# Kernel optimization log

Measured on AMD Instinct MI355X. Metric: run time of the kernel, lower is better.

Reference implementation:

```python
import jax, jax.numpy as jnp
import numpy as np

L, H, E, V, BS = 12, 12, 768, 50257, 1024  # layers, heads, n_embd, vocab, block_size
B, T = 2, 1024
D = E // H


def setup_inputs() -> dict:
    key = jax.random.key(0)
    ks = jax.random.split(key, 10)
    s = 0.02
    d = {}
    d["idx"] = jax.random.randint(ks[0], (B, T), 0, V)
    d["targets"] = jax.random.randint(ks[1], (B, T), 0, V)
    # embeddings (wte tied with lm_head)
    d["wte"] = (jax.random.normal(ks[2], (V, E)) * s).astype(jnp.float32)
    d["wpe"] = (jax.random.normal(ks[3], (BS, E)) * s).astype(jnp.float32)
    # stacked per-layer params; Linear weights stored [in, out] (= torch W.T)
    d["ln1_w"] = jnp.ones((L, E), jnp.float32)
    d["ln1_b"] = jnp.zeros((L, E), jnp.float32)
    d["attn_w"] = (jax.random.normal(ks[4], (L, E, 3 * E)) * s).astype(jnp.float32)
    d["attn_b"] = jnp.zeros((L, 3 * E), jnp.float32)
    d["proj_w"] = (jax.random.normal(ks[5], (L, E, E)) * s).astype(jnp.float32)
    d["proj_b"] = jnp.zeros((L, E), jnp.float32)
    d["ln2_w"] = jnp.ones((L, E), jnp.float32)
    d["ln2_b"] = jnp.zeros((L, E), jnp.float32)
    d["fc_w"] = (jax.random.normal(ks[6], (L, E, 4 * E)) * s).astype(jnp.float32)
    d["fc_b"] = jnp.zeros((L, 4 * E), jnp.float32)
    d["fcproj_w"] = (jax.random.normal(ks[7], (L, 4 * E, E)) * s).astype(jnp.float32)
    d["fcproj_b"] = jnp.zeros((L, E), jnp.float32)
    d["lnf_w"] = jnp.ones((E,), jnp.float32)
    d["lnf_b"] = jnp.zeros((E,), jnp.float32)
    return d


def _ln(x, w, b, eps=1e-5):
    m = jnp.mean(x, -1, keepdims=True)
    v = jnp.mean(jnp.square(x - m), -1, keepdims=True)
    return (x - m) * jax.lax.rsqrt(v + eps) * w + b


def _block(x, p, mask):
    l1w, l1b, aw, ab, pw, pb, l2w, l2b, fw, fb, fpw, fpb = p
    Bx, Tx, C = x.shape
    # causal self-attention (explicit QK^T + mask + softmax + AV, as in source)
    qkv = _ln(x, l1w, l1b) @ aw + ab                       # [B,T,3E]
    q, k, v = jnp.split(qkv, 3, axis=-1)
    q = q.reshape(Bx, Tx, H, D).transpose(0, 2, 1, 3)       # [B,H,T,D]
    k = k.reshape(Bx, Tx, H, D).transpose(0, 2, 1, 3)
    v = v.reshape(Bx, Tx, H, D).transpose(0, 2, 1, 3)
    att = jnp.einsum('bhqd,bhkd->bhqk', q, k) * (1.0 / np.sqrt(D))
    att = jnp.where(mask, att, -jnp.inf)
    att = jax.nn.softmax(att, axis=-1)
    y = jnp.einsum('bhqk,bhkd->bhqd', att, v)
    y = y.transpose(0, 2, 1, 3).reshape(Bx, Tx, C)
    x = x + y @ pw + pb
    # MLP with tanh-approx GELU
    h = jax.nn.gelu(_ln(x, l2w, l2b) @ fw + fb, approximate=True)
    x = x + h @ fpw + fpb
    return x


def reference(idx, targets, wte, wpe, ln1_w, ln1_b, attn_w, attn_b, proj_w, proj_b,
              ln2_w, ln2_b, fc_w, fc_b, fcproj_w, fcproj_b, lnf_w, lnf_b):
    Tq = idx.shape[1]
    x = wte[idx] + wpe[:Tq]                                 # [B,T,E]
    mask = jnp.tril(jnp.ones((Tq, Tq), dtype=bool))

    def step(x, p):
        return _block(x, p, mask), None

    layer_params = (ln1_w, ln1_b, attn_w, attn_b, proj_w, proj_b,
                    ln2_w, ln2_b, fc_w, fc_b, fcproj_w, fcproj_b)
    x, _ = jax.lax.scan(step, x, layer_params)
    x = _ln(x, lnf_w, lnf_b)
    logits = x @ wte.T                                      # tied lm_head, [B,T,V]
    logp = jax.nn.log_softmax(logits, axis=-1)
    nll = -jnp.take_along_axis(logp, targets[..., None], axis=-1)[..., 0]
    loss = jnp.mean(nll)
    return logits, loss
```

## Files before the change

### kernel.cpp

```cpp
#include <hip/hip_runtime.h>
#include <hip/hip_bf16.h>
#include <math.h>

#define LNUM 12
#define HNUM 12
#define EDIM 768
#define VDIM 50257
#define BDIM 2
#define TDIM 1024
#define BT (BDIM*TDIM)
#define E3 (3*EDIM)
#define E4 (4*EDIM)
#define NPB (2*((VDIM+127)/128))

typedef __bf16 bf16x8 __attribute__((ext_vector_type(8)));
typedef __bf16 bf16x4 __attribute__((ext_vector_type(4)));
typedef float f32x4 __attribute__((ext_vector_type(4)));

__device__ __forceinline__ float gelu_f(float x) {
    float u = 0.7978845608028654f * (x + 0.044715f * x * x * x);
    return 0.5f * x * (1.0f + tanhf(u));
}

__device__ __forceinline__ void gl16(const void* g, void* l) {
    __builtin_amdgcn_global_load_lds(
        (const __attribute__((address_space(1))) unsigned int*)g,
        (__attribute__((address_space(3))) unsigned int*)l,
        16, 0, 0);
}

__global__ __launch_bounds__(256) void embed_kernel(
    const int* __restrict__ idx, const float* __restrict__ wte,
    const float* __restrict__ wpe, float* __restrict__ x)
{
    const int row = blockIdx.x;
    const int t = row % TDIM;
    const int tok = idx[row];
    const float* we = wte + (size_t)tok * EDIM;
    const float* pe = wpe + (size_t)t * EDIM;
    float* xr = x + (size_t)row * EDIM;
    for (int e = threadIdx.x; e < EDIM; e += 256) xr[e] = we[e] + pe[e];
}

__global__ __launch_bounds__(256) void ln_kernel(
    const float* __restrict__ in, const float* __restrict__ w,
    const float* __restrict__ b, __bf16* __restrict__ out)
{
    const int row = blockIdx.x * 4 + (threadIdx.x >> 6);
    const int lane = threadIdx.x & 63;
    const float4* xr = (const float4*)(in + (size_t)row * EDIM);
    float4 a0 = xr[lane], a1 = xr[64 + lane], a2 = xr[128 + lane];
    float s = a0.x + a0.y + a0.z + a0.w + a1.x + a1.y + a1.z + a1.w
            + a2.x + a2.y + a2.z + a2.w;
    #pragma unroll
    for (int off = 32; off; off >>= 1) s += __shfl_xor(s, off);
    const float mean = s * (1.0f / EDIM);
    float4 d0 = make_float4(a0.x - mean, a0.y - mean, a0.z - mean, a0.w - mean);
    float4 d1 = make_float4(a1.x - mean, a1.y - mean, a1.z - mean, a1.w - mean);
    float4 d2 = make_float4(a2.x - mean, a2.y - mean, a2.z - mean, a2.w - mean);
    float v = d0.x*d0.x + d0.y*d0.y + d0.z*d0.z + d0.w*d0.w
            + d1.x*d1.x + d1.y*d1.y + d1.z*d1.z + d1.w*d1.w
            + d2.x*d2.x + d2.y*d2.y + d2.z*d2.z + d2.w*d2.w;
    #pragma unroll
    for (int off = 32; off; off >>= 1) v += __shfl_xor(v, off);
    const float inv = rsqrtf(v * (1.0f / EDIM) + 1e-5f);
    const float4* w4 = (const float4*)w;
    const float4* b4 = (const float4*)b;
    __bf16* orow = out + (size_t)row * EDIM;
    #pragma unroll
    for (int c = 0; c < 3; ++c) {
        float4 dd = c == 0 ? d0 : (c == 1 ? d1 : d2);
        float4 ww = w4[c * 64 + lane], bb = b4[c * 64 + lane];
        bf16x4 o;
        o[0] = (__bf16)(dd.x * inv * ww.x + bb.x);
        o[1] = (__bf16)(dd.y * inv * ww.y + bb.y);
        o[2] = (__bf16)(dd.z * inv * ww.z + bb.z);
        o[3] = (__bf16)(dd.w * inv * ww.w + bb.w);
        *(bf16x4*)(orow + c * 256 + lane * 4) = o;
    }
}

__global__ __launch_bounds__(256) void convt_kernel(
    const float* __restrict__ in, __bf16* __restrict__ out, int K, int N)
{
    in  += (size_t)blockIdx.z * K * N;
    out += (size_t)blockIdx.z * K * N;
    __shared__ float t[32][33];
    const int n0 = blockIdx.x * 32, k0 = blockIdx.y * 32;
    const int tx = threadIdx.x & 31, ty = threadIdx.x >> 5;
    #pragma unroll
    for (int r = ty; r < 32; r += 8)
        t[r][tx] = in[(size_t)(k0 + r) * N + n0 + tx];
    __syncthreads();
    #pragma unroll
    for (int r = ty; r < 32; r += 8)
        out[(size_t)(n0 + r) * K + k0 + tx] = (__bf16)t[tx][r];
}

__global__ __launch_bounds__(256) void cvt_kernel(
    const float* __restrict__ in, __bf16* __restrict__ out, long n4)
{
    for (long i = blockIdx.x * 256L + threadIdx.x; i < n4; i += (long)gridDim.x * 256L) {
        float4 v = ((const float4*)in)[i];
        out[i * 4 + 0] = (__bf16)v.x;
        out[i * 4 + 1] = (__bf16)v.y;
        out[i * 4 + 2] = (__bf16)v.z;
        out[i * 4 + 3] = (__bf16)v.w;
    }
}

template<int BM, int BN, int BK, bool BIAS, bool GELU_, bool RES_, bool OUTBF, bool NGUARD, bool LOGITS>
__global__ __launch_bounds__(256, 2) void mgemm(
    const __bf16* __restrict__ A, const __bf16* __restrict__ Bt,
    const float* __restrict__ bias, const float* __restrict__ res,
    void* __restrict__ Cout, float* __restrict__ part, int M, int N, int K)
{
    constexpr int WM = BM / 2, WN = BN / 2;
    constexpr int FM = WM / 16, FN = WN / 16;
    constexpr int KS = BK / 32;
    constexpr int TBA = BM * BK * 2;
    constexpr int TBB = BN * BK * 2;
    constexpr int rA = TBA / 4096, rB = TBB / 4096;
    constexpr int RPI = 2048 / BK;
    constexpr int CPR = BK / 8;
    __shared__ __align__(16) __bf16 As[3 * BM * BK];
    __shared__ __align__(16) __bf16 Bs[3 * BN * BK];
    const int tid = threadIdx.x;
    const int lane = tid & 63;
    const int wave = tid >> 6;
    const int wr = wave >> 1, wc = wave & 1;

    int bm, bn;
    if (LOGITS) {
        const int wg = blockIdx.x;
        bm = (wg >> 3) & 7;
        bn = (wg & 7) + ((wg >> 6) << 3);
        if (bn * BN >= N) return;
    } else { bm = blockIdx.y; bn = blockIdx.x; }
    const int m0 = bm * BM;
    const int n0 = bn * BN;

    const int srow = tid / CPR;
    const int skey = (BK == 32) ? ((srow >> 1) & 3) : (srow & 7);
    const int c0 = (tid % CPR) ^ skey;

    const __bf16* gA = A + (size_t)(m0 + srow) * K + c0 * 8;
    const __bf16* gB[rB];
    #pragma unroll
    for (int r = 0; r < rB; ++r) {
        int nr = n0 + srow + r * RPI;
        if (NGUARD) nr = nr < N ? nr : N - 1;
        gB[r] = Bt + (size_t)nr * K + c0 * 8;
    }

    const int fr = lane & 15;
    const int g = lane >> 4;
    const int fkey = (BK == 32) ? ((fr >> 1) & 3) : (fr & 7);

    f32x4 acc[FM][FN];
    #pragma unroll
    for (int i = 0; i < FM; i++)
        #pragma unroll
        for (int j = 0; j < FN; j++) acc[i][j] = (f32x4){0.f, 0.f, 0.f, 0.f};

    const int nt = K / BK;

    auto stage = [&](int kk, int b) {
        #pragma unroll
        for (int r = 0; r < rA; ++r)
            gl16(gA + (size_t)r * RPI * K + kk, (char*)As + b * TBA + r * 4096 + tid * 16);
        #pragma unroll
        for (int r = 0; r < rB; ++r)
            gl16(gB[r] + kk, (char*)Bs + b * TBB + r * 4096 + tid * 16);
    };

    stage(0, 0);
    if (nt > 1) stage(BK, 1);

    int b0 = 0, b1 = 1, b2 = 2;
    for (int t = 0; t < nt; ++t) {
        if (t + 1 < nt) {
            static_assert(rA + rB == 4 || rA + rB == 6, "vmcnt literal");
            if constexpr (rA + rB == 4) asm volatile("s_waitcnt vmcnt(4)" ::: "memory");
            else                        asm volatile("s_waitcnt vmcnt(6)" ::: "memory");
        } else {
            asm volatile("s_waitcnt vmcnt(0)" ::: "memory");
        }
        asm volatile("s_barrier" ::: "memory");
        if (t + 2 < nt) stage((t + 2) * BK, b2);

        const char* pa = (const char*)As + b0 * TBA;
        const char* pb = (const char*)Bs + b0 * TBB;
        bf16x8 af[FM][KS], bfr[FN][KS];
        #pragma unroll
        for (int i = 0; i < FM; i++)
            #pragma unroll
            for (int kc = 0; kc < KS; kc++)
                af[i][kc] = *(const bf16x8*)(pa + (wr * WM + i * 16 + fr) * (2 * BK)
                                                + (((kc * 4 + g) ^ fkey) << 4));
        #pragma unroll
        for (int j = 0; j < FN; j++)
            #pragma unroll
            for (int kc = 0; kc < KS; kc++)
                bfr[j][kc] = *(const bf16x8*)(pb + (wc * WN + j * 16 + fr) * (2 * BK)
                                                 + (((kc * 4 + g) ^ fkey) << 4));
        #pragma unroll
        for (int kc = 0; kc < KS; kc++)
            #pragma unroll
            for (int i = 0; i < FM; i++)
                #pragma unroll
                for (int j = 0; j < FN; j++)
                    acc[i][j] = __builtin_amdgcn_mfma_f32_16x16x32_bf16(af[i][kc], bfr[j][kc], acc[i][j], 0, 0, 0);
        const int tmp = b0; b0 = b1; b1 = b2; b2 = tmp;
    }

    const int crow = g * 4;
    if (LOGITS) {
        const int bn2 = bn * 2 + wc;
        #pragma unroll
        for (int i = 0; i < FM; i++) {
            #pragma unroll
            for (int r = 0; r < 4; r++) {
                const int m = m0 + wr * WM + i * 16 + crow + r;
                float se = 0.f;
                #pragma unroll
                for (int j = 0; j < FN; j++) {
                    const int n = n0 + wc * WN + j * 16 + fr;
                    if (n < N) {
                        float v = acc[i][j][r];
                        ((float*)Cout)[(size_t)m * N + n] = v;
                        se += __expf(v);
                    }
                }
                se += __shfl_xor(se, 1); se += __shfl_xor(se, 2);
                se += __shfl_xor(se, 4); se += __shfl_xor(se, 8);
                if (fr == 0) part[(size_t)m * NPB + bn2] = se;
            }
        }
    } else {
        #pragma unroll
        for (int i = 0; i < FM; i++) {
            #pragma unroll
            for (int r = 0; r < 4; r++) {
                const int m = m0 + wr * WM + i * 16 + crow + r;
                #pragma unroll
                for (int j = 0; j < FN; j++) {
                    const int n = n0 + wc * WN + j * 16 + fr;
                    if (!NGUARD || n < N) {
                        float v = acc[i][j][r];
                        if (BIAS) v += bias[n];
                        if (GELU_) v = gelu_f(v);
                        if (RES_) v += res[(size_t)m * N + n];
                        if (OUTBF) ((__bf16*)Cout)[(size_t)m * N + n] = (__bf16)v;
                        else       ((float*)Cout)[(size_t)m * N + n] = v;
                    }
                }
            }
        }
    }
}

__global__ __launch_bounds__(256) void fattn_kernel(
    const __bf16* __restrict__ qkv, __bf16* __restrict__ y)
{
    const int bq = blockIdx.x, h = blockIdx.y, b = blockIdx.z;
    const int tid = threadIdx.x, lane = tid & 63, w = tid >> 6;
    const int fr = lane & 15, g = lane >> 4;

    __shared__ __align__(16) __bf16 Ks[64 * 64];
    __shared__ __align__(16) __bf16 Vt[64 * 64];
    __shared__ __align__(16) __bf16 Ps[4][16 * 64];

    const __bf16* base = qkv + (size_t)b * TDIM * E3;
    const int q0w = bq * 64 + w * 16;

    bf16x8 qf[2];
    {
        const __bf16* qp = base + (size_t)(q0w + fr) * E3 + h * 64 + g * 8;
        qf[0] = *(const bf16x8*)qp;
        qf[1] = *(const bf16x8*)(qp + 32);
    }

    const int r0 = tid >> 3, ch = tid & 7;
    bf16x8 kr[2], vr[2];

    #pragma unroll
    for (int it = 0; it < 2; ++it) {
        const int row = it * 32 + r0;
        const __bf16* gp = base + (size_t)row * E3 + EDIM + h * 64 + ch * 8;
        kr[it] = *(const bf16x8*)gp;
        vr[it] = *(const bf16x8*)(gp + EDIM);
    }
    #pragma unroll
    for (int it = 0; it < 2; ++it) {
        const int row = it * 32 + r0;
        *(bf16x8*)(Ks + row * 64 + ((ch ^ (row & 7)) << 3)) = kr[it];
        #pragma unroll
        for (int j = 0; j < 8; ++j) {
            const int d = ch * 8 + j;
            const int key = ((d >> 3) ^ d) & 7;
            Vt[d * 64 + ((((row >> 3) ^ key) << 3) + (row & 7))] = vr[it][j];
        }
    }
    __syncthreads();

    float m[4] = {-1e30f, -1e30f, -1e30f, -1e30f};
    float l[4] = {0.f, 0.f, 0.f, 0.f};
    f32x4 acc[4];
    #pragma unroll
    for (int jd = 0; jd < 4; ++jd) acc[jd] = (f32x4){0.f, 0.f, 0.f, 0.f};

    for (int kt = 0; kt <= bq; ++kt) {
        if (kt < bq) {
            const int k1 = (kt + 1) * 64;
            #pragma unroll
            for (int it = 0; it < 2; ++it) {
                const int row = it * 32 + r0;
                const __bf16* gp = base + (size_t)(k1 + row) * E3 + EDIM + h * 64 + ch * 8;
                kr[it] = *(const bf16x8*)gp;
                vr[it] = *(const bf16x8*)(gp + EDIM);
            }
        }

        const int k0 = kt * 64;
        f32x4 s[4];
        #pragma unroll
        for (int jf = 0; jf < 4; ++jf) {
            const int krow = jf * 16 + fr;
            f32x4 sv = (f32x4){0.f, 0.f, 0.f, 0.f};
            #pragma unroll
            for (int kc = 0; kc < 2; ++kc) {
                bf16x8 kf = *(const bf16x8*)(Ks + krow * 64 + (((kc * 4 + g) ^ (fr & 7)) << 3));
                sv = __builtin_amdgcn_mfma_f32_16x16x32_bf16(qf[kc], kf, sv, 0, 0, 0);
            }
            s[jf] = sv;
        }
        #pragma unroll
        for (int jf = 0; jf < 4; ++jf)
            #pragma unroll
            for (int r = 0; r < 4; ++r) s[jf][r] *= 0.125f;
        if (kt == bq) {
            #pragma unroll
            for (int jf = 0; jf < 4; ++jf) {
                const int k = k0 + jf * 16 + fr;
                #pragma unroll
                for (int r = 0; r < 4; ++r) {
                    const int q = q0w + g * 4 + r;
                    if (k > q) s[jf][r] = -1e30f;
                }
            }
        }

        #pragma unroll
        for (int r = 0; r < 4; ++r) {
            float mx = fmaxf(fmaxf(s[0][r], s[1][r]), fmaxf(s[2][r], s[3][r]));
            mx = fmaxf(mx, __shfl_xor(mx, 1));
            mx = fmaxf(mx, __shfl_xor(mx, 2));
            mx = fmaxf(mx, __shfl_xor(mx, 4));
            mx = fmaxf(mx, __shfl_xor(mx, 8));
            const float mn = fmaxf(m[r], mx);
            const float sc2 = __expf(m[r] - mn);
            m[r] = mn;
            float rs = 0.f;
            #pragma unroll
            for (int jf = 0; jf < 4; ++jf) {
                const float p = __expf(s[jf][r] - mn);
                s[jf][r] = p;
                rs += p;
            }
            rs += __shfl_xor(rs, 1);
            rs += __shfl_xor(rs, 2);
            rs += __shfl_xor(rs, 4);
            rs += __shfl_xor(rs, 8);
            l[r] = l[r] * sc2 + rs;
            #pragma unroll
            for (int jd = 0; jd < 4; ++jd) acc[jd][r] *= sc2;
        }

        __bf16* pw = &Ps[w][0];
        #pragma unroll
        for (int jf = 0; jf < 4; ++jf) {
            const int chp = jf * 2 + (fr >> 3);
            #pragma unroll
            for (int r = 0; r < 4; ++r) {
                const int row = g * 4 + r;
                pw[row * 64 + (((chp ^ (row & 7)) << 3) + (fr & 7))] = (__bf16)s[jf][r];
            }
        }
        asm volatile("s_waitcnt lgkmcnt(0)" ::: "memory");
        bf16x8 pa[2];
        #pragma unroll
        for (int kc = 0; kc < 2; ++kc)
            pa[kc] = *(const bf16x8*)(pw + fr * 64 + (((kc * 4 + g) ^ (fr & 7)) << 3));

        #pragma unroll
        for (int jd = 0; jd < 4; ++jd) {
            const int d = jd * 16 + fr;
            const int key = ((d >> 3) ^ d) & 7;
            #pragma unroll
            for (int kc = 0; kc < 2; ++kc) {
                bf16x8 vf = *(const bf16x8*)(Vt + d * 64 + (((kc * 4 + g) ^ key) << 3));
                acc[jd] = __builtin_amdgcn_mfma_f32_16x16x32_bf16(pa[kc], vf, acc[jd], 0, 0, 0);
            }
        }

        if (kt < bq) {
            __syncthreads();
            #pragma unroll
            for (int it = 0; it < 2; ++it) {
                const int row = it * 32 + r0;
                *(bf16x8*)(Ks + row * 64 + ((ch ^ (row & 7)) << 3)) = kr[it];
                #pragma unroll
                for (int j = 0; j < 8; ++j) {
                    const int d = ch * 8 + j;
                    const int key = ((d >> 3) ^ d) & 7;
                    Vt[d * 64 + ((((row >> 3) ^ key) << 3) + (row & 7))] = vr[it][j];
                }
            }
            __syncthreads();
        }
    }

    #pragma unroll
    for (int r = 0; r < 4; ++r) {
        const float inv = 1.0f / l[r];
        const int q = q0w + g * 4 + r;
        __bf16* yp = y + ((size_t)(b * TDIM + q)) * EDIM + h * 64;
        #pragma unroll
        for (int jd = 0; jd < 4; ++jd)
            yp[jd * 16 + fr] = (__bf16)(acc[jd][r] * inv);
    }
}

__global__ __launch_bounds__(256) void lsefin_kernel(
    const float* __restrict__ part, const float* __restrict__ logits,
    const int* __restrict__ targets, float* __restrict__ rr)
{
    const int row = blockIdx.x, tid = threadIdx.x;
    float s = 0.f;
    for (int j = tid; j < NPB; j += 256) s += part[(size_t)row * NPB + j];
    #pragma unroll
    for (int off = 32; off; off >>= 1) s += __shfl_xor(s, off);
    __shared__ float red[4];
    if ((tid & 63) == 0) red[tid >> 6] = s;
    __syncthreads();
    if (tid == 0) {
        float S = red[0] + red[1] + red[2] + red[3];
        rr[row] = logf(S) - logits[(size_t)row * VDIM + targets[row]];
    }
}

__global__ __launch_bounds__(256) void loss_reduce_kernel(
    const float* __restrict__ rr, float* __restrict__ out)
{
    const int tid = threadIdx.x;
    float s = 0.f;
    for (int i = tid; i < BT; i += 256) s += rr[i];
    #pragma unroll
    for (int off = 32; off; off >>= 1) s += __shfl_xor(s, off);
    __shared__ float red[4];
    if ((tid & 63) == 0) red[tid >> 6] = s;
    __syncthreads();
    if (tid == 0) out[0] = (red[0] + red[1] + red[2] + red[3]) * (1.0f / BT);
}

extern "C" void kernel_launch(void* const* d_in, const int* in_sizes, int n_in,
                              void* d_out, int out_size, void* d_ws, size_t ws_size,
                              hipStream_t stream)
{
    const int*   idx     = (const int*)d_in[0];
    const int*   targets = (const int*)d_in[1];
    const float* wte     = (const float*)d_in[2];
    const float* wpe     = (const float*)d_in[3];
    const float* ln1_w   = (const float*)d_in[4];
    const float* ln1_b   = (const float*)d_in[5];
    const float* attn_w  = (const float*)d_in[6];
    const float* attn_b  = (const float*)d_in[7];
    const float* proj_w  = (const float*)d_in[8];
    const float* proj_b  = (const float*)d_in[9];
    const float* ln2_w   = (const float*)d_in[10];
    const float* ln2_b   = (const float*)d_in[11];
    const float* fc_w    = (const float*)d_in[12];
    const float* fc_b    = (const float*)d_in[13];
    const float* fcp_w   = (const float*)d_in[14];
    const float* fcp_b   = (const float*)d_in[15];
    const float* lnf_w   = (const float*)d_in[16];
    const float* lnf_b   = (const float*)d_in[17];

    float* logits = (float*)d_out;

    const size_t slq = (size_t)EDIM * E3, slp = (size_t)EDIM * EDIM;
    const size_t slf = (size_t)EDIM * E4, slfp = (size_t)E4 * EDIM;

    char* wp = (char*)d_ws;
    float*  x     = (float*)wp;   wp += (size_t)BT * EDIM * 4;
    __bf16* qkvb  = (__bf16*)wp;  wp += (size_t)BT * E3 * 2;
    __bf16* xnbf  = (__bf16*)wp;  wp += (size_t)BT * EDIM * 2;
    __bf16* ybf   = (__bf16*)wp;  wp += (size_t)BT * EDIM * 2;
    __bf16* hbf   = (__bf16*)wp;  wp += (size_t)BT * E4 * 2;
    __bf16* wteb  = (__bf16*)wp;  wp += (size_t)VDIM * EDIM * 2;
    float*  part  = (float*)wp;   wp += (size_t)BT * NPB * 4;
    float*  rr    = (float*)wp;   wp += (size_t)BT * 4;
    __bf16* wqkvb = (__bf16*)wp;

    const size_t wbytes_all = (slq + slp + slf + slfp) * 2 * LNUM;
    const size_t used = (size_t)(wp - (char*)d_ws);
    const bool big = ws_size >= used + wbytes_all;
    const size_t L = big ? LNUM : 1;
    __bf16* wprjb = wqkvb + slq * L;
    __bf16* wfcb  = wprjb + slp * L;
    __bf16* wfpb  = wfcb  + slf * L;

    embed_kernel<<<BT, 256, 0, stream>>>(idx, wte, wpe, x);
    cvt_kernel<<<2048, 256, 0, stream>>>(wte, wteb, (long)VDIM * EDIM / 4);

    if (big) {
        convt_kernel<<<dim3(E3 / 32, EDIM / 32, LNUM), 256, 0, stream>>>(attn_w, wqkvb, EDIM, E3);
        convt_kernel<<<dim3(EDIM / 32, EDIM / 32, LNUM), 256, 0, stream>>>(proj_w, wprjb, EDIM, EDIM);
        convt_kernel<<<dim3(E4 / 32, EDIM / 32, LNUM), 256, 0, stream>>>(fc_w, wfcb, EDIM, E4);
        convt_kernel<<<dim3(EDIM / 32, E4 / 32, LNUM), 256, 0, stream>>>(fcp_w, wfpb, E4, EDIM);
    }

    for (int l = 0; l < LNUM; ++l) {
        const __bf16* wq = wqkvb + (big ? (size_t)l * slq : 0);
        const __bf16* wpj = wprjb + (big ? (size_t)l * slp : 0);
        const __bf16* wf = wfcb + (big ? (size_t)l * slf : 0);
        const __bf16* wfp = wfpb + (big ? (size_t)l * slfp : 0);

        ln_kernel<<<BT / 4, 256, 0, stream>>>(x, ln1_w + (size_t)l * EDIM,
                                              ln1_b + (size_t)l * EDIM, xnbf);
        if (!big)
            convt_kernel<<<dim3(E3 / 32, EDIM / 32), 256, 0, stream>>>(
                attn_w + (size_t)l * slq, (__bf16*)wq, EDIM, E3);
        mgemm<128, 128, 32, true, false, false, true, false, false>
            <<<dim3(E3 / 128, BT / 128), 256, 0, stream>>>(
            xnbf, wq, attn_b + (size_t)l * E3, nullptr, qkvb, nullptr, BT, E3, EDIM);
        fattn_kernel<<<dim3(TDIM / 64, HNUM, BDIM), 256, 0, stream>>>(qkvb, ybf);
        if (!big)
            convt_kernel<<<dim3(EDIM / 32, EDIM / 32), 256, 0, stream>>>(
                proj_w + (size_t)l * slp, (__bf16*)wpj, EDIM, EDIM);
        mgemm<64, 64, 64, true, false, true, false, false, false>
            <<<dim3(EDIM / 64, BT / 64), 256, 0, stream>>>(
            ybf, wpj, proj_b + (size_t)l * EDIM, x, x, nullptr, BT, EDIM, EDIM);
        ln_kernel<<<BT / 4, 256, 0, stream>>>(x, ln2_w + (size_t)l * EDIM,
                                              ln2_b + (size_t)l * EDIM, xnbf);
        if (!big)
            convt_kernel<<<dim3(E4 / 32, EDIM / 32), 256, 0, stream>>>(
                fc_w + (size_t)l * slf, (__bf16*)wf, EDIM, E4);
        mgemm<128, 128, 32, true, true, false, true, false, false>
            <<<dim3(E4 / 128, BT / 128), 256, 0, stream>>>(
            xnbf, wf, fc_b + (size_t)l * E4, nullptr, hbf, nullptr, BT, E4, EDIM);
        if (!big)
            convt_kernel<<<dim3(EDIM / 32, E4 / 32), 256, 0, stream>>>(
                fcp_w + (size_t)l * slfp, (__bf16*)wfp, E4, EDIM);
        mgemm<64, 64, 64, true, false, true, false, false, false>
            <<<dim3(EDIM / 64, BT / 64), 256, 0, stream>>>(
            hbf, wfp, fcp_b + (size_t)l * EDIM, x, x, nullptr, BT, EDIM, E4);
    }

    ln_kernel<<<BT / 4, 256, 0, stream>>>(x, lnf_w, lnf_b, xnbf);
    mgemm<256, 128, 32, false, false, false, false, true, true>
        <<<dim3(64 * 50), 256, 0, stream>>>(
        xnbf, wteb, nullptr, nullptr, logits, part, BT, VDIM, EDIM);
    lsefin_kernel<<<BT, 256, 0, stream>>>(part, logits, targets, rr);
    loss_reduce_kernel<<<1, 256, 0, stream>>>(rr, logits + (size_t)BT * VDIM);
}
```

Baseline: 2.256 ms.

## Add single-wave 128x64 GEMM for QKV and FC, reverse attention block order

Adds a new GEMM kernel that uses one 64-thread wave per 128x64 output tile, with triple-buffered direct-to-LDS loads and a swizzled layout. It replaces the 256-thread 128x128 GEMM for the QKV and FC projections. The aim is more, smaller blocks for better CU occupancy and load balance on these N=2304/3072 shapes, at the cost of less LDS reuse per block. The flash-attention grid is also reversed so the heaviest causal query blocks are scheduled first, which should reduce tail imbalance.

Result: slower. 2.446 ms (+8.4%).

```diff
diff --git a/kernel.cpp b/kernel.cpp
--- a/kernel.cpp
+++ b/kernel.cpp
@@ -106,6 +106,82 @@
         out[i * 4 + 1] = (__bf16)v.y;
         out[i * 4 + 2] = (__bf16)v.z;
         out[i * 4 + 3] = (__bf16)v.w;
+    }
+}
+
+template<bool GELU_>
+__global__ __launch_bounds__(64) void wgemm(
+    const __bf16* __restrict__ A, const __bf16* __restrict__ Bt,
+    const float* __restrict__ bias, __bf16* __restrict__ Cout,
+    int M, int N, int K)
+{
+    __shared__ __align__(16) __bf16 As[3 * 128 * 32];
+    __shared__ __align__(16) __bf16 Bs[3 * 64 * 32];
+    const int lane = threadIdx.x;
+    const int m0 = blockIdx.y * 128, n0 = blockIdx.x * 64;
+
+    const int srow = lane >> 2;
+    const int c0 = (lane & 3) ^ ((srow >> 1) & 3);
+    const __bf16* gA = A + (size_t)(m0 + srow) * K + c0 * 8;
+    const __bf16* gB = Bt + (size_t)(n0 + srow) * K + c0 * 8;
+
+    const int fr = lane & 15, g = lane >> 4;
+    const int slot = ((g ^ ((fr >> 1) & 3)) << 4);
+
+    f32x4 acc[8][4];
+    #pragma unroll
+    for (int i = 0; i < 8; ++i)
+        #pragma unroll
+        for (int j = 0; j < 4; ++j) acc[i][j] = (f32x4){0.f, 0.f, 0.f, 0.f};
+
+    const int nt = K >> 5;
+    auto stage = [&](int kk, int b) {
+        #pragma unroll
+        for (int r = 0; r < 8; ++r)
+            gl16(gA + (size_t)(r * 16) * K + kk, (char*)As + b * 8192 + r * 1024 + lane * 16);
+        #pragma unroll
+        for (int r = 0; r < 4; ++r)
+            gl16(gB + (size_t)(r * 16) * K + kk, (char*)Bs + b * 4096 + r * 1024 + lane * 16);
+    };
+
+    stage(0, 0);
+    stage(32, 1);
+
+    int b0 = 0, b1 = 1, b2 = 2;
+    for (int t = 0; t < nt; ++t) {
+        if (t + 1 < nt) asm volatile("s_waitcnt vmcnt(12)" ::: "memory");
+        else            asm volatile("s_waitcnt vmcnt(0)"  ::: "memory");
+        if (t + 2 < nt) stage((t + 2) << 5, b2);
+        const char* pa = (const char*)As + b0 * 8192;
+        const char* pb = (const char*)Bs + b0 * 4096;
+        bf16x8 bfr[4];
+        #pragma unroll
+        for (int j = 0; j < 4; ++j)
+            bfr[j] = *(const bf16x8*)(pb + (j * 16 + fr) * 64 + slot);
+        #pragma unroll
+        for (int i = 0; i < 8; ++i) {
+            bf16x8 af = *(const bf16x8*)(pa + (i * 16 + fr) * 64 + slot);
+            #pragma unroll
+            for (int j = 0; j < 4; ++j)
+                acc[i][j] = __builtin_amdgcn_mfma_f32_16x16x32_bf16(af, bfr[j], acc[i][j], 0, 0, 0);
+        }
+        const int tmp = b0; b0 = b1; b1 = b2; b2 = tmp;
+    }
+
+    const int crow = g * 4;
+    #pragma unroll
+    for (int i = 0; i < 8; ++i) {
+        #pragma unroll
+        for (int r = 0; r < 4; ++r) {
+            const int m = m0 + i * 16 + crow + r;
+            #pragma unroll
+            for (int j = 0; j < 4; ++j) {
+                const int n = n0 + j * 16 + fr;
+                float v = acc[i][j][r] + bias[n];
+                if (GELU_) v = gelu_f(v);
+                Cout[(size_t)m * N + n] = (__bf16)v;
+            }
+        }
     }
 }
 
@@ -263,7 +339,8 @@
 __global__ __launch_bounds__(256) void fattn_kernel(
     const __bf16* __restrict__ qkv, __bf16* __restrict__ y)
 {
-    const int bq = blockIdx.x, h = blockIdx.y, b = blockIdx.z;
+    const int bq = gridDim.x - 1 - blockIdx.x;
+    const int h = blockIdx.y, b = blockIdx.z;
     const int tid = threadIdx.x, lane = tid & 63, w = tid >> 6;
     const int fr = lane & 15, g = lane >> 4;
 
@@ -532,9 +609,8 @@
         if (!big)
             convt_kernel<<<dim3(E3 / 32, EDIM / 32), 256, 0, stream>>>(
                 attn_w + (size_t)l * slq, (__bf16*)wq, EDIM, E3);
-        mgemm<128, 128, 32, true, false, false, true, false, false>
-            <<<dim3(E3 / 128, BT / 128), 256, 0, stream>>>(
-            xnbf, wq, attn_b + (size_t)l * E3, nullptr, qkvb, nullptr, BT, E3, EDIM);
+        wgemm<false><<<dim3(E3 / 64, BT / 128), 64, 0, stream>>>(
+            xnbf, wq, attn_b + (size_t)l * E3, qkvb, BT, E3, EDIM);
         fattn_kernel<<<dim3(TDIM / 64, HNUM, BDIM), 256, 0, stream>>>(qkvb, ybf);
         if (!big)
             convt_kernel<<<dim3(EDIM / 32, EDIM / 32), 256, 0, stream>>>(
@@ -547,9 +623,8 @@
         if (!big)
             convt_kernel<<<dim3(E4 / 32, EDIM / 32), 256, 0, stream>>>(
                 fc_w + (size_t)l * slf, (__bf16*)wf, EDIM, E4);
-        mgemm<128, 128, 32, true, true, false, true, false, false>
-            <<<dim3(E4 / 128, BT / 128), 256, 0, stream>>>(
-            xnbf, wf, fc_b + (size_t)l * E4, nullptr, hbf, nullptr, BT, E4, EDIM);
+        wgemm<true><<<dim3(E4 / 64, BT / 128), 64, 0, stream>>>(
+            xnbf, wf, fc_b + (size_t)l * E4, hbf, BT, E4, EDIM);
         if (!big)
             convt_kernel<<<dim3(EDIM / 32, E4 / 32), 256, 0, stream>>>(
                 fcp_w + (size_t)l * slfp, (__bf16*)wfp, E4, EDIM);
```
